# Performance work log

Hardware: AMD Instinct MI355X
Metric: run time of the kernel (lower is better)

## Reference

```python
import jax, jax.numpy as jnp
import numpy as np

N = 262144          # num_nodes
H = 512             # hidden_dim
NH = 8              # num_heads
HD = H // NH        # head_dim = 64
C = 32              # num_centroids
MOM = 0.99          # centroid EMA momentum
LN_EPS = 1e-5


def setup_inputs() -> dict:
    key = jax.random.key(0)
    ks = jax.random.split(key, 12)
    s = 0.02
    return {
        "x": jax.random.normal(ks[0], (N, H), dtype=jnp.float32),
        "centroids": jax.random.normal(ks[1], (C, H), dtype=jnp.float32),
        "Wq": jax.random.normal(ks[2], (H, H), dtype=jnp.float32) * s,
        "bq": jnp.zeros((H,), jnp.float32),
        "Wk": jax.random.normal(ks[3], (H, H), dtype=jnp.float32) * s,
        "bk": jnp.zeros((H,), jnp.float32),
        "Wv": jax.random.normal(ks[4], (H, H), dtype=jnp.float32) * s,
        "bv": jnp.zeros((H,), jnp.float32),
        "Wo": jax.random.normal(ks[5], (H, H), dtype=jnp.float32) * s,
        "bo": jnp.zeros((H,), jnp.float32),
        "ln_w": jnp.ones((H,), jnp.float32),
        "ln_b": jnp.zeros((H,), jnp.float32),
    }


def _update_centroids(x, centroids):
    # nearest-centroid assignment (argmin of squared euclidean == argmin of cdist)
    d2 = (
        jnp.sum(x * x, axis=1, keepdims=True)
        - 2.0 * (x @ centroids.T)
        + jnp.sum(centroids * centroids, axis=1)[None, :]
    )  # [N, C]
    assign = jnp.argmin(d2, axis=1)  # [N]
    sums = jax.ops.segment_sum(x, assign, num_segments=C)           # [C, H]
    counts = jax.ops.segment_sum(jnp.ones((x.shape[0],), x.dtype), assign, num_segments=C)  # [C]
    means = sums / jnp.maximum(counts, 1.0)[:, None]
    updated = jnp.where(
        (counts > 0)[:, None], MOM * centroids + (1.0 - MOM) * means, centroids
    )
    # torch update is in no_grad; value changes but grads flow to the param identity-style
    return centroids + jax.lax.stop_gradient(updated - centroids)


def reference(x, centroids, Wq, bq, Wk, bk, Wv, bv, Wo, bo, ln_w, ln_b):
    residual = x
    centroids = _update_centroids(x, centroids)  # training-mode EMA k-means step

    q = (x @ Wq + bq).reshape(-1, NH, HD)           # [N, nh, hd]
    k = (centroids @ Wk + bk).reshape(C, NH, HD)    # [C, nh, hd]
    v = (centroids @ Wv + bv).reshape(C, NH, HD)

    scores = jnp.einsum("nhd,chd->nhc", q, k) / np.sqrt(HD).astype(np.float32)
    attn = jax.nn.softmax(scores, axis=-1)          # dropout = identity (eval semantics)
    ctx = jnp.einsum("nhc,chd->nhd", attn, v).reshape(-1, H)

    out = ctx @ Wo + bo
    y = out + residual
    mu = jnp.mean(y, axis=-1, keepdims=True)
    var = jnp.mean((y - mu) ** 2, axis=-1, keepdims=True)
    return (y - mu) * jax.lax.rsqrt(var + LN_EPS) * ln_w + ln_b
```

## Files before the change

kernel.cpp:

```cpp
#include <hip/hip_runtime.h>

#define NN 262144
#define HH 512
#define CC 32
#define MOMF 0.99f

#define WS_SUMS   0
#define WS_COUNTS 131072
#define WS_UPD    131328
#define WS_KBUF   147712
#define WS_VBUF   164096
#define WS_SB     180480
#define WS_MT     180736
#define WS_PT     246272
#define WS_ASSIGN 279040

typedef __attribute__((ext_vector_type(8))) short s8v;
typedef __attribute__((ext_vector_type(4))) float f4v;
typedef __attribute__((ext_vector_type(4))) unsigned int u4v;

static __device__ __forceinline__ unsigned short f2bf(float f) {
  unsigned int u = __float_as_uint(f);
  u += 0x7FFFu + ((u >> 16) & 1u);
  return (unsigned short)(u >> 16);
}
static __device__ __forceinline__ unsigned int pk2bf(float a, float b) {
  return (unsigned int)f2bf(a) | ((unsigned int)f2bf(b) << 16);
}
#define EL4(v, k) ((k) == 0 ? (v).x : (k) == 1 ? (v).y : (k) == 2 ? (v).z : (v).w)

__global__ __launch_bounds__(256) void k_asn(const float* __restrict__ x,
                                             const float* __restrict__ cent,
                                             unsigned char* __restrict__ sag) {
  __shared__ __align__(16) unsigned char smem[34432];
  unsigned short* clbf = (unsigned short*)smem;
  float* cnS = (float*)(smem + 33280);
  float* scratch = (float*)(smem + 33408);

  const int tid = threadIdx.x;
  const int w = tid >> 6, l = tid & 63;
  const int l16 = l & 15, g = l >> 4;

  for (int i = tid * 8; i < CC * HH; i += 256 * 8) {
    float4 a = *(const float4*)&cent[i];
    float4 b = *(const float4*)&cent[i + 4];
    const int row = i >> 9, col = i & 511;
    u4v p;
    p[0] = pk2bf(a.x, a.y); p[1] = pk2bf(a.z, a.w);
    p[2] = pk2bf(b.x, b.y); p[3] = pk2bf(b.z, b.w);
    *(u4v*)((unsigned char*)clbf + row * 1040 + col * 2) = p;
  }
  {
    const int c = tid >> 3, kk = tid & 7;
    float p = 0.f;
    for (int m = 0; m < 64; ++m) { float v = cent[c * HH + kk + 8 * m]; p += v * v; }
    scratch[tid] = p;
  }
  __syncthreads();
  if (tid < CC) {
    float s = 0.f;
#pragma unroll
    for (int m = 0; m < 8; ++m) s += scratch[tid * 8 + m];
    cnS[tid] = s;
  }
  __syncthreads();

  float cnr[8];
#pragma unroll
  for (int tc = 0; tc < 2; ++tc)
#pragma unroll
    for (int r = 0; r < 4; ++r) cnr[tc * 4 + r] = cnS[tc * 16 + 4 * g + r];

  for (int pass = 0; pass < 2; ++pass) {
    const int nodeloc = pass * 64 + w * 16 + l16;
    const float* xr = x + ((size_t)blockIdx.x * 128 + nodeloc) * HH;
    f4v acc[2];
    acc[0] = (f4v){0.f, 0.f, 0.f, 0.f};
    acc[1] = (f4v){0.f, 0.f, 0.f, 0.f};
    float4 pa[2][4], pb[2][4];
#pragma unroll
    for (int k = 0; k < 4; ++k) {
      pa[0][k] = *(const float4*)&xr[k * 32 + g * 8];
      pb[0][k] = *(const float4*)&xr[k * 32 + g * 8 + 4];
    }
#pragma unroll
    for (int c4 = 0; c4 < 4; ++c4) {
      const int cur = c4 & 1, nxt = cur ^ 1;
      if (c4 < 3) {
#pragma unroll
        for (int k = 0; k < 4; ++k) {
          const int kk = (c4 + 1) * 4 + k;
          pa[nxt][k] = *(const float4*)&xr[kk * 32 + g * 8];
          pb[nxt][k] = *(const float4*)&xr[kk * 32 + g * 8 + 4];
        }
      }
#pragma unroll
      for (int k = 0; k < 4; ++k) {
        const int kk = c4 * 4 + k;
        float4 xa = pa[cur][k], xb = pb[cur][k];
        s8v bfrag;
        bfrag[0] = (short)f2bf(xa.x); bfrag[1] = (short)f2bf(xa.y);
        bfrag[2] = (short)f2bf(xa.z); bfrag[3] = (short)f2bf(xa.w);
        bfrag[4] = (short)f2bf(xb.x); bfrag[5] = (short)f2bf(xb.y);
        bfrag[6] = (short)f2bf(xb.z); bfrag[7] = (short)f2bf(xb.w);
#pragma unroll
        for (int tc = 0; tc < 2; ++tc) {
          s8v afrag = *(const s8v*)((unsigned char*)clbf +
                                    (tc * 16 + l16) * 1040 + kk * 64 + g * 16);
          acc[tc] = __builtin_amdgcn_mfma_f32_16x16x32_bf16(afrag, bfrag, acc[tc], 0, 0, 0);
        }
      }
    }
    float bv = 3.4e38f; int bi = 0;
#pragma unroll
    for (int tc = 0; tc < 2; ++tc)
#pragma unroll
      for (int r = 0; r < 4; ++r) {
        const int c = tc * 16 + 4 * g + r;
        const float v = cnr[tc * 4 + r] - 2.f * acc[tc][r];
        if (v < bv) { bv = v; bi = c; }
      }
#pragma unroll
    for (int m = 16; m <= 32; m <<= 1) {
      const float ov = __shfl_xor(bv, m);
      const int oi = __shfl_xor(bi, m);
      if (ov < bv || (ov == bv && oi < bi)) { bv = ov; bi = oi; }
    }
    if (l < 16) sag[(size_t)blockIdx.x * 128 + nodeloc] = (unsigned char)bi;
  }
}

__global__ __launch_bounds__(256) void k_sum(const float* __restrict__ x,
                                             const unsigned char* __restrict__ sag,
                                             float* __restrict__ gsums,
                                             float* __restrict__ gcounts) {
  __shared__ __align__(16) unsigned char xt[32768];
  const int tid = threadIdx.x;
  const int w = tid >> 6, l = tid & 63;
  const int l16 = l & 15, g = l >> 4;
  const int q = tid & 7, cc = tid >> 3;
  const size_t node0 = (size_t)blockIdx.x * 512;
  const unsigned char* sab = sag + node0;

  f4v acc[8][2];
#pragma unroll
  for (int ct = 0; ct < 8; ++ct) {
    acc[ct][0] = (f4v){0.f, 0.f, 0.f, 0.f};
    acc[ct][1] = (f4v){0.f, 0.f, 0.f, 0.f};
  }

  for (int step = 0; step < 16; ++step) {
    float4 r[4][4];
    const float* xs = x + (node0 + step * 32 + q * 4) * HH + cc * 16;
#pragma unroll
    for (int nn = 0; nn < 4; ++nn)
#pragma unroll
      for (int f = 0; f < 4; ++f)
        r[nn][f] = *(const float4*)&xs[nn * HH + f * 4];
    const uint2 awv = *(const uint2*)(sab + step * 32 + 8 * g);
    __syncthreads();
#pragma unroll
    for (int j = 0; j < 16; ++j) {
      uint2 p;
      p.x = pk2bf(EL4(r[0][j >> 2], j & 3), EL4(r[1][j >> 2], j & 3));
      p.y = pk2bf(EL4(r[2][j >> 2], j & 3), EL4(r[3][j >> 2], j & 3));
      *(uint2*)(xt + (cc * 16 + j) * 64 + q * 8) = p;
    }
    __syncthreads();
    s8v oh0, oh1;
#pragma unroll
    for (int j = 0; j < 8; ++j) {
      const unsigned a = ((j < 4 ? awv.x >> (8 * j) : awv.y >> (8 * (j - 4)))) & 255u;
      oh0[j] = (a == (unsigned)l16) ? (short)0x3F80 : (short)0;
      oh1[j] = (a == (unsigned)(16 + l16)) ? (short)0x3F80 : (short)0;
    }
#pragma unroll
    for (int ct = 0; ct < 8; ++ct) {
      s8v af = *(const s8v*)(xt + (w * 128 + ct * 16 + l16) * 64 + g * 16);
      acc[ct][0] = __builtin_amdgcn_mfma_f32_16x16x32_bf16(af, oh0, acc[ct][0], 0, 0, 0);
      acc[ct][1] = __builtin_amdgcn_mfma_f32_16x16x32_bf16(af, oh1, acc[ct][1], 0, 0, 0);
    }
  }

  const int pb = blockIdx.x & 7;
#pragma unroll
  for (int ct = 0; ct < 8; ++ct)
#pragma unroll
    for (int tc = 0; tc < 2; ++tc) {
      const int c = tc * 16 + l16;
      const int xcol = w * 128 + ct * 16 + 4 * g;
#pragma unroll
      for (int r = 0; r < 4; ++r)
        atomicAdd(&gsums[pb * 16384 + c * HH + xcol + r], acc[ct][tc][r]);
    }

  if (w == 0 && l < CC) {
    int cnt = 0;
    for (int i = 0; i < 512; i += 4) {
      const unsigned wd = *(const unsigned*)(sab + i);
      cnt += (int)((wd & 255u) == (unsigned)l) + (int)(((wd >> 8) & 255u) == (unsigned)l) +
             (int)(((wd >> 16) & 255u) == (unsigned)l) + (int)(((wd >> 24) & 255u) == (unsigned)l);
    }
    atomicAdd(&gcounts[pb * 32 + l], (float)cnt);
  }
}

__global__ void k_upd(const float* __restrict__ cent, const float* __restrict__ sums,
                      const float* __restrict__ counts, float* __restrict__ upd) {
  const int i = blockIdx.x * 256 + threadIdx.x;
  const int c = i >> 9;
  float s = 0.f, cnt = 0.f;
#pragma unroll
  for (int b = 0; b < 8; ++b) { s += sums[b * 16384 + i]; cnt += counts[b * 32 + c]; }
  const float mean = s / fmaxf(cnt, 1.f);
  upd[i] = (cnt > 0.f) ? (MOMF * cent[i] + (1.f - MOMF) * mean) : cent[i];
}

__global__ void k_kv(const float* __restrict__ upd,
                     const float* __restrict__ Wk, const float* __restrict__ bk,
                     const float* __restrict__ Wv, const float* __restrict__ bv,
                     float* __restrict__ kbuf, float* __restrict__ vbuf) {
  const int o = blockIdx.x * 256 + threadIdx.x;
  const int sel = o >> 14;
  const int idx = o & 16383;
  const int c = idx >> 9, j = idx & 511;
  const float* W = sel ? Wv : Wk;
  const float* b = sel ? bv : bk;
  const float* u = upd + c * HH;
  float s = b[j];
  for (int i = 0; i < HH; ++i) s += u[i] * W[i * HH + j];
  (sel ? vbuf : kbuf)[idx] = s;
}

__global__ void k_msp(const float* __restrict__ Wq, const float* __restrict__ bq,
                      const float* __restrict__ kbuf, const float* __restrict__ vbuf,
                      const float* __restrict__ Wo, const float* __restrict__ bo,
                      unsigned short* __restrict__ Mt, float* __restrict__ sb,
                      unsigned short* __restrict__ Pt) {
  const int b = blockIdx.x, t = threadIdx.x;
  const float scale = 0.125f;
  if (b < 512) {
    const int o = b * 256 + t;
    const int hc = o >> 9, i = o & 511;
    const int h = hc >> 5, c = hc & 31;
    const float* wq = Wq + i * HH + h * 64;
    const float* kr = kbuf + c * HH + h * 64;
    float s = 0.f;
#pragma unroll
    for (int d = 0; d < 64; ++d) s += wq[d] * kr[d];
    Mt[(i >> 5) * 8192 + hc * 32 + (i & 31)] = f2bf(s * scale);
  } else if (b < 1024) {
    const int o = b - 512;
    const int hc = t;
    const int h = hc >> 5, c = hc & 31;
    const float* vr = vbuf + c * HH + h * 64;
    const float* wo = Wo + h * 64 * HH + o;
    float s = 0.f;
#pragma unroll
    for (int d = 0; d < 64; ++d) s += vr[d] * wo[d * HH];
    Pt[h * 16384 + o * 32 + (hc & 31)] = f2bf(s + bo[o] * scale);
  } else if (t < 256) {
    const int h = t >> 5, c = t & 31;
    const float* kr = kbuf + c * HH + h * 64;
    const float* bqp = bq + h * 64;
    float s = 0.f;
#pragma unroll
    for (int d = 0; d < 64; ++d) s += bqp[d] * kr[d];
    sb[t] = s * scale;
  }
}

__global__ __launch_bounds__(256, 2) void k_main(
    const float* __restrict__ x, const unsigned short* __restrict__ Mt,
    const float* __restrict__ sb, const unsigned short* __restrict__ Pt,
    const float* __restrict__ lnw, const float* __restrict__ lnb,
    float* __restrict__ y) {
  __shared__ __align__(16) unsigned char smem[40960];
  float* yb = (float*)smem;
  const unsigned char* Mtb = (const unsigned char*)Mt;
  const unsigned char* Ptb = (const unsigned char*)Pt;
  const int tid = threadIdx.x;
  const int w = tid >> 6, l = tid & 63;
  const int l16 = l & 15, g = l >> 4;
  const size_t n0 = (size_t)blockIdx.x * 64;
  const size_t xrow = n0 + w * 16 + l16;
  const float* xr = x + xrow * HH;

  {
    const unsigned char* src = Mtb + tid * 64;
    u4v r0 = *(const u4v*)(src), r1 = *(const u4v*)(src + 16);
    u4v r2 = *(const u4v*)(src + 32), r3 = *(const u4v*)(src + 48);
    unsigned char* dst = smem + tid * 80;
    *(u4v*)(dst) = r0; *(u4v*)(dst + 16) = r1;
    *(u4v*)(dst + 32) = r2; *(u4v*)(dst + 48) = r3;
  }
  float4 xa_c = *(const float4*)&xr[g * 8];
  float4 xb_c = *(const float4*)&xr[g * 8 + 4];
  __syncthreads();

  f4v acc1[16];
#pragma unroll
  for (int tc = 0; tc < 16; ++tc)
    acc1[tc] = *(const f4v*)&sb[tc * 16 + 4 * g];

#pragma unroll
  for (int kk = 0; kk < 16; ++kk) {
    const int cur = (kk & 1) * 20480, nxt = ((kk + 1) & 1) * 20480;
    u4v r0, r1, r2, r3;
    float4 xa_n, xb_n;
    {
      const unsigned char* src =
          (kk < 15) ? (Mtb + (kk + 1) * 16384 + tid * 64) : (Ptb + tid * 64);
      r0 = *(const u4v*)(src); r1 = *(const u4v*)(src + 16);
      r2 = *(const u4v*)(src + 32); r3 = *(const u4v*)(src + 48);
    }
    if (kk < 15) {
      xa_n = *(const float4*)&xr[(kk + 1) * 32 + g * 8];
      xb_n = *(const float4*)&xr[(kk + 1) * 32 + g * 8 + 4];
    }
    s8v bfrag;
    bfrag[0] = (short)f2bf(xa_c.x); bfrag[1] = (short)f2bf(xa_c.y);
    bfrag[2] = (short)f2bf(xa_c.z); bfrag[3] = (short)f2bf(xa_c.w);
    bfrag[4] = (short)f2bf(xb_c.x); bfrag[5] = (short)f2bf(xb_c.y);
    bfrag[6] = (short)f2bf(xb_c.z); bfrag[7] = (short)f2bf(xb_c.w);
#pragma unroll
    for (int tc = 0; tc < 16; ++tc) {
      s8v afrag = *(const s8v*)(smem + cur + (tc * 16 + l16) * 80 + g * 16);
      acc1[tc] = __builtin_amdgcn_mfma_f32_16x16x32_bf16(afrag, bfrag, acc1[tc], 0, 0, 0);
    }
    {
      unsigned char* dst = smem + nxt + tid * 80;
      *(u4v*)(dst) = r0; *(u4v*)(dst + 16) = r1;
      *(u4v*)(dst + 32) = r2; *(u4v*)(dst + 48) = r3;
    }
    __syncthreads();
    if (kk < 15) { xa_c = xa_n; xb_c = xb_n; }
  }

  unsigned int apk[16][2];
#pragma unroll
  for (int h = 0; h < 8; ++h) {
    f4v s0 = acc1[2 * h], s1 = acc1[2 * h + 1];
    float m = fmaxf(fmaxf(fmaxf(s0[0], s0[1]), fmaxf(s0[2], s0[3])),
                    fmaxf(fmaxf(s1[0], s1[1]), fmaxf(s1[2], s1[3])));
    m = fmaxf(m, __shfl_xor(m, 16));
    m = fmaxf(m, __shfl_xor(m, 32));
    float e0 = __expf(s0[0] - m), e1 = __expf(s0[1] - m);
    float e2 = __expf(s0[2] - m), e3 = __expf(s0[3] - m);
    float e4 = __expf(s1[0] - m), e5 = __expf(s1[1] - m);
    float e6 = __expf(s1[2] - m), e7 = __expf(s1[3] - m);
    float sum = ((e0 + e1) + (e2 + e3)) + ((e4 + e5) + (e6 + e7));
    sum += __shfl_xor(sum, 16);
    sum += __shfl_xor(sum, 32);
    const float inv = 1.f / sum;
    apk[2 * h][0] = pk2bf(e0 * inv, e1 * inv);
    apk[2 * h][1] = pk2bf(e2 * inv, e3 * inv);
    apk[2 * h + 1][0] = pk2bf(e4 * inv, e5 * inv);
    apk[2 * h + 1][1] = pk2bf(e6 * inv, e7 * inv);
  }

  f4v acc2[32];
#pragma unroll
  for (int to = 0; to < 32; ++to) acc2[to] = (f4v){0.f, 0.f, 0.f, 0.f};

#pragma unroll
  for (int s = 0; s < 16; ++s) {
    const int cur = (s & 1) * 20480, nxt = ((s + 1) & 1) * 20480;
    const int h = s >> 1, half = s & 1;
    u4v r0, r1, r2, r3;
    if (s < 15) {
      const unsigned char* src = Ptb + (s + 1) * 16384 + tid * 64;
      r0 = *(const u4v*)(src); r1 = *(const u4v*)(src + 16);
      r2 = *(const u4v*)(src + 32); r3 = *(const u4v*)(src + 48);
    }
    unsigned int dw[4];
#pragma unroll
    for (int d = 0; d < 4; ++d) {
      const int gsrc = 2 * (g & 1) + (d >> 1);
      const int src = l16 + 16 * gsrc;
      unsigned int t0 = (unsigned int)__shfl((int)apk[2 * h][d & 1], src, 64);
      unsigned int t1 = (unsigned int)__shfl((int)apk[2 * h + 1][d & 1], src, 64);
      dw[d] = (g < 2) ? t0 : t1;
    }
    u4v bu; bu[0] = dw[0]; bu[1] = dw[1]; bu[2] = dw[2]; bu[3] = dw[3];
    s8v bfrag = __builtin_bit_cast(s8v, bu);
#pragma unroll
    for (int tl = 0; tl < 16; ++tl) {
      s8v afrag = *(const s8v*)(smem + cur + (tl * 16 + l16) * 80 + g * 16);
      acc2[half * 16 + tl] =
          __builtin_amdgcn_mfma_f32_16x16x32_bf16(afrag, bfrag, acc2[half * 16 + tl], 0, 0, 0);
    }
    if (s < 15) {
      unsigned char* dst = smem + nxt + tid * 80;
      *(u4v*)(dst) = r0; *(u4v*)(dst + 16) = r1;
      *(u4v*)(dst + 32) = r2; *(u4v*)(dst + 48) = r3;
    }
    __syncthreads();
  }

  float s1 = 0.f, s2 = 0.f;
#pragma unroll
  for (int to = 0; to < 32; ++to) {
    float4 xv = *(const float4*)&xr[to * 16 + 4 * g];
    acc2[to][0] += xv.x; acc2[to][1] += xv.y;
    acc2[to][2] += xv.z; acc2[to][3] += xv.w;
    s1 += (acc2[to][0] + acc2[to][1]) + (acc2[to][2] + acc2[to][3]);
    s2 += (acc2[to][0] * acc2[to][0] + acc2[to][1] * acc2[to][1]) +
          (acc2[to][2] * acc2[to][2] + acc2[to][3] * acc2[to][3]);
  }
  s1 += __shfl_xor(s1, 16); s2 += __shfl_xor(s2, 16);
  s1 += __shfl_xor(s1, 32); s2 += __shfl_xor(s2, 32);
  const float mean = s1 * (1.f / 512.f);
  const float var = s2 * (1.f / 512.f) - mean * mean;
  const float rstd = rsqrtf(var + 1e-5f);
#pragma unroll
  for (int to = 0; to < 32; ++to) {
    float4 wv = *(const float4*)&lnw[to * 16 + 4 * g];
    float4 bv = *(const float4*)&lnb[to * 16 + 4 * g];
    acc2[to][0] = (acc2[to][0] - mean) * rstd * wv.x + bv.x;
    acc2[to][1] = (acc2[to][1] - mean) * rstd * wv.y + bv.y;
    acc2[to][2] = (acc2[to][2] - mean) * rstd * wv.z + bv.z;
    acc2[to][3] = (acc2[to][3] - mean) * rstd * wv.w + bv.w;
  }

  const int prow = tid >> 7;
  const int pc = (tid & 127) * 4;
  for (int j = 0; j < 4; ++j) {
    __syncthreads();
    if (w == j) {
#pragma unroll
      for (int to = 0; to < 32; ++to)
        *(f4v*)&yb[l16 * 520 + to * 16 + 4 * g] = acc2[to];
    }
    __syncthreads();
#pragma unroll
    for (int p = 0; p < 8; ++p)
      *(float4*)&y[(n0 + j * 16 + p * 2 + prow) * HH + pc] =
          *(const float4*)&yb[(p * 2 + prow) * 520 + pc];
  }
}

extern "C" void kernel_launch(void* const* d_in, const int* in_sizes, int n_in,
                              void* d_out, int out_size, void* d_ws, size_t ws_size,
                              hipStream_t stream) {
  const float* x    = (const float*)d_in[0];
  const float* cent = (const float*)d_in[1];
  const float* Wq   = (const float*)d_in[2];
  const float* bq   = (const float*)d_in[3];
  const float* Wk   = (const float*)d_in[4];
  const float* bk   = (const float*)d_in[5];
  const float* Wv   = (const float*)d_in[6];
  const float* bv   = (const float*)d_in[7];
  const float* Wo   = (const float*)d_in[8];
  const float* bo   = (const float*)d_in[9];
  const float* lnw  = (const float*)d_in[10];
  const float* lnb  = (const float*)d_in[11];
  float* ws = (float*)d_ws;
  float* y  = (float*)d_out;

  hipMemsetAsync(ws, 0, (8 * 16384 + 8 * 32) * sizeof(float), stream);
  k_asn<<<2048, 256, 0, stream>>>(x, cent, (unsigned char*)(ws + WS_ASSIGN));
  k_sum<<<512, 256, 0, stream>>>(x, (const unsigned char*)(ws + WS_ASSIGN),
                                 ws + WS_SUMS, ws + WS_COUNTS);
  k_upd<<<64, 256, 0, stream>>>(cent, ws + WS_SUMS, ws + WS_COUNTS, ws + WS_UPD);
  k_kv<<<128, 256, 0, stream>>>(ws + WS_UPD, Wk, bk, Wv, bv,
                                ws + WS_KBUF, ws + WS_VBUF);
  k_msp<<<1025, 256, 0, stream>>>(Wq, bq, ws + WS_KBUF, ws + WS_VBUF, Wo, bo,
                                  (unsigned short*)(ws + WS_MT), ws + WS_SB,
                                  (unsigned short*)(ws + WS_PT));
  k_main<<<4096, 256, 0, stream>>>(x, (const unsigned short*)(ws + WS_MT),
                                   ws + WS_SB, (const unsigned short*)(ws + WS_PT),
                                   lnw, lnb, y);
}
```

Measured before the change: 877.9 us.

## Fuse centroid assignment and segment-sum kernels into one pass

Merges the nearest-centroid assignment kernel and the segment-sum kernel into a single kernel. Each block of 512 nodes computes assignments chunk by chunk into shared memory and then accumulates per-centroid sums from that same chunk of x. This removes one launch and the global round trip for the assignment bytes, and rereads each chunk of x while it is likely still in cache. In exchange it runs with 512 blocks instead of 2048 for the assignment phase and uses about 66 KB of shared memory per block, which lowers occupancy and adds extra barriers.

```diff
diff --git a/kernel.cpp b/kernel.cpp
--- a/kernel.cpp
+++ b/kernel.cpp
@@ -13,7 +13,6 @@
 #define WS_SB     180480
 #define WS_MT     180736
 #define WS_PT     246272
-#define WS_ASSIGN 279040
 
 typedef __attribute__((ext_vector_type(8))) short s8v;
 typedef __attribute__((ext_vector_type(4))) float f4v;
@@ -29,13 +28,16 @@
 }
 #define EL4(v, k) ((k) == 0 ? (v).x : (k) == 1 ? (v).y : (k) == 2 ? (v).z : (v).w)
 
-__global__ __launch_bounds__(256) void k_asn(const float* __restrict__ x,
+__global__ __launch_bounds__(256) void k_km2(const float* __restrict__ x,
                                              const float* __restrict__ cent,
-                                             unsigned char* __restrict__ sag) {
-  __shared__ __align__(16) unsigned char smem[34432];
+                                             float* __restrict__ gsums,
+                                             float* __restrict__ gcounts) {
+  __shared__ __align__(16) unsigned char smem[66688];
   unsigned short* clbf = (unsigned short*)smem;
   float* cnS = (float*)(smem + 33280);
-  float* scratch = (float*)(smem + 33408);
+  unsigned char* saL = smem + 33408;
+  unsigned char* xt = smem + 33920;
+  float* scratch = (float*)(smem + 33920);
 
   const int tid = threadIdx.x;
   const int w = tid >> 6, l = tid & 63;
@@ -71,76 +73,8 @@
 #pragma unroll
     for (int r = 0; r < 4; ++r) cnr[tc * 4 + r] = cnS[tc * 16 + 4 * g + r];
 
-  for (int pass = 0; pass < 2; ++pass) {
-    const int nodeloc = pass * 64 + w * 16 + l16;
-    const float* xr = x + ((size_t)blockIdx.x * 128 + nodeloc) * HH;
-    f4v acc[2];
-    acc[0] = (f4v){0.f, 0.f, 0.f, 0.f};
-    acc[1] = (f4v){0.f, 0.f, 0.f, 0.f};
-    float4 pa[2][4], pb[2][4];
-#pragma unroll
-    for (int k = 0; k < 4; ++k) {
-      pa[0][k] = *(const float4*)&xr[k * 32 + g * 8];
-      pb[0][k] = *(const float4*)&xr[k * 32 + g * 8 + 4];
-    }
-#pragma unroll
-    for (int c4 = 0; c4 < 4; ++c4) {
-      const int cur = c4 & 1, nxt = cur ^ 1;
-      if (c4 < 3) {
-#pragma unroll
-        for (int k = 0; k < 4; ++k) {
-          const int kk = (c4 + 1) * 4 + k;
-          pa[nxt][k] = *(const float4*)&xr[kk * 32 + g * 8];
-          pb[nxt][k] = *(const float4*)&xr[kk * 32 + g * 8 + 4];
-        }
-      }
-#pragma unroll
-      for (int k = 0; k < 4; ++k) {
-        const int kk = c4 * 4 + k;
-        float4 xa = pa[cur][k], xb = pb[cur][k];
-        s8v bfrag;
-        bfrag[0] = (short)f2bf(xa.x); bfrag[1] = (short)f2bf(xa.y);
-        bfrag[2] = (short)f2bf(xa.z); bfrag[3] = (short)f2bf(xa.w);
-        bfrag[4] = (short)f2bf(xb.x); bfrag[5] = (short)f2bf(xb.y);
-        bfrag[6] = (short)f2bf(xb.z); bfrag[7] = (short)f2bf(xb.w);
-#pragma unroll
-        for (int tc = 0; tc < 2; ++tc) {
-          s8v afrag = *(const s8v*)((unsigned char*)clbf +
-                                    (tc * 16 + l16) * 1040 + kk * 64 + g * 16);
-          acc[tc] = __builtin_amdgcn_mfma_f32_16x16x32_bf16(afrag, bfrag, acc[tc], 0, 0, 0);
-        }
-      }
-    }
-    float bv = 3.4e38f; int bi = 0;
-#pragma unroll
-    for (int tc = 0; tc < 2; ++tc)
-#pragma unroll
-      for (int r = 0; r < 4; ++r) {
-        const int c = tc * 16 + 4 * g + r;
-        const float v = cnr[tc * 4 + r] - 2.f * acc[tc][r];
-        if (v < bv) { bv = v; bi = c; }
-      }
-#pragma unroll
-    for (int m = 16; m <= 32; m <<= 1) {
-      const float ov = __shfl_xor(bv, m);
-      const int oi = __shfl_xor(bi, m);
-      if (ov < bv || (ov == bv && oi < bi)) { bv = ov; bi = oi; }
-    }
-    if (l < 16) sag[(size_t)blockIdx.x * 128 + nodeloc] = (unsigned char)bi;
-  }
-}
-
-__global__ __launch_bounds__(256) void k_sum(const float* __restrict__ x,
-                                             const unsigned char* __restrict__ sag,
-                                             float* __restrict__ gsums,
-                                             float* __restrict__ gcounts) {
-  __shared__ __align__(16) unsigned char xt[32768];
-  const int tid = threadIdx.x;
-  const int w = tid >> 6, l = tid & 63;
-  const int l16 = l & 15, g = l >> 4;
+  const size_t node0 = (size_t)blockIdx.x * 512;
   const int q = tid & 7, cc = tid >> 3;
-  const size_t node0 = (size_t)blockIdx.x * 512;
-  const unsigned char* sab = sag + node0;
 
   f4v acc[8][2];
 #pragma unroll
@@ -149,37 +83,101 @@
     acc[ct][1] = (f4v){0.f, 0.f, 0.f, 0.f};
   }
 
-  for (int step = 0; step < 16; ++step) {
-    float4 r[4][4];
-    const float* xs = x + (node0 + step * 32 + q * 4) * HH + cc * 16;
-#pragma unroll
-    for (int nn = 0; nn < 4; ++nn)
-#pragma unroll
-      for (int f = 0; f < 4; ++f)
-        r[nn][f] = *(const float4*)&xs[nn * HH + f * 4];
-    const uint2 awv = *(const uint2*)(sab + step * 32 + 8 * g);
-    __syncthreads();
-#pragma unroll
-    for (int j = 0; j < 16; ++j) {
-      uint2 p;
-      p.x = pk2bf(EL4(r[0][j >> 2], j & 3), EL4(r[1][j >> 2], j & 3));
-      p.y = pk2bf(EL4(r[2][j >> 2], j & 3), EL4(r[3][j >> 2], j & 3));
-      *(uint2*)(xt + (cc * 16 + j) * 64 + q * 8) = p;
-    }
-    __syncthreads();
-    s8v oh0, oh1;
-#pragma unroll
-    for (int j = 0; j < 8; ++j) {
-      const unsigned a = ((j < 4 ? awv.x >> (8 * j) : awv.y >> (8 * (j - 4)))) & 255u;
-      oh0[j] = (a == (unsigned)l16) ? (short)0x3F80 : (short)0;
-      oh1[j] = (a == (unsigned)(16 + l16)) ? (short)0x3F80 : (short)0;
-    }
-#pragma unroll
-    for (int ct = 0; ct < 8; ++ct) {
-      s8v af = *(const s8v*)(xt + (w * 128 + ct * 16 + l16) * 64 + g * 16);
-      acc[ct][0] = __builtin_amdgcn_mfma_f32_16x16x32_bf16(af, oh0, acc[ct][0], 0, 0, 0);
-      acc[ct][1] = __builtin_amdgcn_mfma_f32_16x16x32_bf16(af, oh1, acc[ct][1], 0, 0, 0);
-    }
+  for (int chunk = 0; chunk < 8; ++chunk) {
+    {
+      const int nodeloc = chunk * 64 + w * 16 + l16;
+      const float* xr = x + (node0 + nodeloc) * HH;
+      f4v acA[2];
+      acA[0] = (f4v){0.f, 0.f, 0.f, 0.f};
+      acA[1] = (f4v){0.f, 0.f, 0.f, 0.f};
+      float4 pa[2][4], pb[2][4];
+#pragma unroll
+      for (int k = 0; k < 4; ++k) {
+        pa[0][k] = *(const float4*)&xr[k * 32 + g * 8];
+        pb[0][k] = *(const float4*)&xr[k * 32 + g * 8 + 4];
+      }
+#pragma unroll
+      for (int c4 = 0; c4 < 4; ++c4) {
+        const int cur = c4 & 1, nxt = cur ^ 1;
+        if (c4 < 3) {
+#pragma unroll
+          for (int k = 0; k < 4; ++k) {
+            const int kk = (c4 + 1) * 4 + k;
+            pa[nxt][k] = *(const float4*)&xr[kk * 32 + g * 8];
+            pb[nxt][k] = *(const float4*)&xr[kk * 32 + g * 8 + 4];
+          }
+        }
+#pragma unroll
+        for (int k = 0; k < 4; ++k) {
+          const int kk = c4 * 4 + k;
+          float4 xa = pa[cur][k], xb = pb[cur][k];
+          s8v bfrag;
+          bfrag[0] = (short)f2bf(xa.x); bfrag[1] = (short)f2bf(xa.y);
+          bfrag[2] = (short)f2bf(xa.z); bfrag[3] = (short)f2bf(xa.w);
+          bfrag[4] = (short)f2bf(xb.x); bfrag[5] = (short)f2bf(xb.y);
+          bfrag[6] = (short)f2bf(xb.z); bfrag[7] = (short)f2bf(xb.w);
+#pragma unroll
+          for (int tc = 0; tc < 2; ++tc) {
+            s8v afrag = *(const s8v*)((unsigned char*)clbf +
+                                      (tc * 16 + l16) * 1040 + kk * 64 + g * 16);
+            acA[tc] = __builtin_amdgcn_mfma_f32_16x16x32_bf16(afrag, bfrag, acA[tc], 0, 0, 0);
+          }
+        }
+      }
+      float bv = 3.4e38f; int bi = 0;
+#pragma unroll
+      for (int tc = 0; tc < 2; ++tc)
+#pragma unroll
+        for (int r = 0; r < 4; ++r) {
+          const int c = tc * 16 + 4 * g + r;
+          const float v = cnr[tc * 4 + r] - 2.f * acA[tc][r];
+          if (v < bv) { bv = v; bi = c; }
+        }
+#pragma unroll
+      for (int m = 16; m <= 32; m <<= 1) {
+        const float ov = __shfl_xor(bv, m);
+        const int oi = __shfl_xor(bi, m);
+        if (ov < bv || (ov == bv && oi < bi)) { bv = ov; bi = oi; }
+      }
+      if (l < 16) saL[nodeloc] = (unsigned char)bi;
+    }
+    __syncthreads();
+
+#pragma unroll
+    for (int sub = 0; sub < 2; ++sub) {
+      const int step = chunk * 2 + sub;
+      float4 r[4][4];
+      const float* xs = x + (node0 + step * 32 + q * 4) * HH + cc * 16;
+#pragma unroll
+      for (int nn = 0; nn < 4; ++nn)
+#pragma unroll
+        for (int f = 0; f < 4; ++f)
+          r[nn][f] = *(const float4*)&xs[nn * HH + f * 4];
+      const uint2 awv = *(const uint2*)(saL + step * 32 + 8 * g);
+      __syncthreads();
+#pragma unroll
+      for (int j = 0; j < 16; ++j) {
+        uint2 p;
+        p.x = pk2bf(EL4(r[0][j >> 2], j & 3), EL4(r[1][j >> 2], j & 3));
+        p.y = pk2bf(EL4(r[2][j >> 2], j & 3), EL4(r[3][j >> 2], j & 3));
+        *(uint2*)(xt + (cc * 16 + j) * 64 + q * 8) = p;
+      }
+      __syncthreads();
+      s8v oh0, oh1;
+#pragma unroll
+      for (int j = 0; j < 8; ++j) {
+        const unsigned a = ((j < 4 ? awv.x >> (8 * j) : awv.y >> (8 * (j - 4)))) & 255u;
+        oh0[j] = (a == (unsigned)l16) ? (short)0x3F80 : (short)0;
+        oh1[j] = (a == (unsigned)(16 + l16)) ? (short)0x3F80 : (short)0;
+      }
+#pragma unroll
+      for (int ct = 0; ct < 8; ++ct) {
+        s8v af = *(const s8v*)(xt + (w * 128 + ct * 16 + l16) * 64 + g * 16);
+        acc[ct][0] = __builtin_amdgcn_mfma_f32_16x16x32_bf16(af, oh0, acc[ct][0], 0, 0, 0);
+        acc[ct][1] = __builtin_amdgcn_mfma_f32_16x16x32_bf16(af, oh1, acc[ct][1], 0, 0, 0);
+      }
+    }
+    __syncthreads();
   }
 
   const int pb = blockIdx.x & 7;
@@ -197,7 +195,7 @@
   if (w == 0 && l < CC) {
     int cnt = 0;
     for (int i = 0; i < 512; i += 4) {
-      const unsigned wd = *(const unsigned*)(sab + i);
+      const unsigned wd = *(const unsigned*)(saL + i);
       cnt += (int)((wd & 255u) == (unsigned)l) + (int)(((wd >> 8) & 255u) == (unsigned)l) +
              (int)(((wd >> 16) & 255u) == (unsigned)l) + (int)(((wd >> 24) & 255u) == (unsigned)l);
     }
@@ -459,9 +457,7 @@
   float* y  = (float*)d_out;
 
   hipMemsetAsync(ws, 0, (8 * 16384 + 8 * 32) * sizeof(float), stream);
-  k_asn<<<2048, 256, 0, stream>>>(x, cent, (unsigned char*)(ws + WS_ASSIGN));
-  k_sum<<<512, 256, 0, stream>>>(x, (const unsigned char*)(ws + WS_ASSIGN),
-                                 ws + WS_SUMS, ws + WS_COUNTS);
+  k_km2<<<512, 256, 0, stream>>>(x, cent, ws + WS_SUMS, ws + WS_COUNTS);
   k_upd<<<64, 256, 0, stream>>>(cent, ws + WS_SUMS, ws + WS_COUNTS, ws + WS_UPD);
   k_kv<<<128, 256, 0, stream>>>(ws + WS_UPD, Wk, bk, Wv, bv,
                                 ws + WS_KBUF, ws + WS_VBUF);
```

After: 810.1 us. 1.08x faster.
